# Performance work log

Measured on AMD Instinct MI355X. Metric: run time of the kernel, lower is better.

## Reference

```python
import math
import jax, jax.numpy as jnp
from jax import lax
import numpy as np

THETA = 10.0      # spiking threshold
TAU_SR = 10.0     # SRM (psp) alpha-kernel time constant
TAU_REF = 1.0     # refractory alpha-kernel time constant
SCALE_REF = 2.0   # refractory scale (kernel = -scaleRef*theta*alpha)
TAU_RHO = 1.0     # surrogate-gradient width
TS = 1.0          # simulation time step


def _alpha_filter_scan(x, tau, extra_input_fn=None):
    """Causal convolution along last (time) axis with alpha kernel
    k[n] = (n*Ts/tau) * exp(1 - n*Ts/tau)  (k[0] = 0),
    implemented exactly as a 2-state linear recurrence.
    x: [N, C, T] -> out: [N, C, T]."""
    d = jnp.float32(math.exp(-TS / tau))
    c = jnp.float32(math.e * TS / tau)
    xT = jnp.moveaxis(x, -1, 0)  # [T, N, C]

    def step(carry, xt):
        p, a = carry
        a = d * (a + p)          # alpha response from inputs up to t-1
        p = d * p + xt           # pure exponential state
        return (p, a), a * c

    z = jnp.zeros_like(xT[0])
    _, out = lax.scan(step, (z, z), xT)
    return jnp.moveaxis(out, 0, -1)


def psp(x):
    return _alpha_filter_scan(x, TAU_SR)


@jax.custom_vjp
def spike_fn(v):
    # Heaviside threshold on (membrane - theta)
    return (v >= 0).astype(v.dtype)

def _spike_fwd(v):
    return spike_fn(v), v

def _spike_bwd(v, g):
    # SLAYER surrogate gradient: exponential pdf around threshold
    grad = (1.0 / TAU_RHO) * jnp.exp(-jnp.abs(v) / TAU_RHO)
    return (g * grad,)

spike_fn.defvjp(_spike_fwd, _spike_bwd)


def spike_layer(u_in):
    """Threshold-and-refract over time. u_in: [N, C, T] psp potentials.
    Refractory response = -scaleRef*theta * alpha_{tauRef}(past spikes)."""
    d = jnp.float32(math.exp(-TS / TAU_REF))
    c = jnp.float32(math.e * TS / TAU_REF)
    ref_scale = jnp.float32(-SCALE_REF * THETA)
    uT = jnp.moveaxis(u_in, -1, 0)  # [T, N, C]

    def step(carry, ut):
        p, a = carry
        a = d * (a + p)                      # refractory potential at t
        u = ut + c * a                       # membrane potential
        s = spike_fn(u - THETA)              # spikes (0/1)
        p = d * p + ref_scale * s            # inject refractory impulse
        return (p, a), s

    z = jnp.zeros_like(uT[0])
    _, s = lax.scan(step, (z, z), uT)
    return jnp.moveaxis(s, 0, -1)


def setup_inputs() -> dict:
    key = jax.random.key(0)
    k1, k2, k3 = jax.random.split(key, 3)
    N, I, H, O, T = 64, 256, 1024, 18, 500
    # Bernoulli(0.1) input spikes
    spike_input = (jax.random.uniform(k1, (N, I, T)) < 0.1).astype(jnp.float32)
    W1 = jax.random.normal(k2, (H, I), dtype=jnp.float32) * (1.0 / math.sqrt(I))
    W2 = jax.random.normal(k3, (O, H), dtype=jnp.float32) * (1.0 / math.sqrt(H))
    return {"spike_input": spike_input, "W1": W1, "W2": W2}


def reference(spike_input, W1, W2):
    # layer 1: dense (per-timestep linear) -> psp -> spike
    y1 = jnp.einsum('nit,hi->nht', spike_input, W1)
    s1 = spike_layer(psp(y1))
    # layer 2
    y2 = jnp.einsum('nht,oh->not', s1, W2)
    s2 = spike_layer(psp(y2))
    return s2
```

## Files before the change

### kernel.cpp

```cpp
#include <hip/hip_runtime.h>


#define NN 64
#define II 256
#define HH 1024
#define OO 18
#define TT 500

#define D_SR 0.9048374180359595f
#define C_SR 0.27182818284590454f
#define D_RF 0.36787944117144233f
#define C_RF 2.718281828459045f
#define THETA 10.0f
#define REFS (-20.0f)

typedef _Float16 f16;
typedef _Float16 f16x8 __attribute__((ext_vector_type(8)));
typedef float f32x4 __attribute__((ext_vector_type(4)));

__device__ __forceinline__ void gl2lds16(const void* g, void* l) {
    __builtin_amdgcn_global_load_lds(
        (const __attribute__((address_space(1))) void*)g,
        (__attribute__((address_space(3))) void*)l, 16, 0, 0);
}

__launch_bounds__(256)
__global__ void prep_all(const float* __restrict__ X, const float* __restrict__ W1,
                         const float* __restrict__ W2, f16* __restrict__ Xb,
                         f16* __restrict__ W1h, f16* __restrict__ W1l,
                         f16* __restrict__ W2h, f16* __restrict__ W2l) {
    __shared__ float tile[64][65];
    const int b = blockIdx.x;
    const int tid = threadIdx.x;

    if (b < 2048) {
        const int t0 = (b & 7) * 64, i0 = ((b >> 3) & 3) * 64, n = b >> 5;
        const int tx = tid & 63, q = tid >> 6;
        const float* Xn = X + (size_t)n * II * TT;
#pragma unroll 4
        for (int j = 0; j < 16; ++j) {
            int il = j * 4 + q;
            int t = t0 + tx;
            tile[il][tx] = (t < TT) ? Xn[(size_t)(i0 + il) * TT + t] : 0.f;
        }
        __syncthreads();
#pragma unroll 4
        for (int j = 0; j < 16; ++j) {
            int tl = j * 4 + q;
            int t = t0 + tl;
            if (t < TT)
                Xb[((size_t)n * TT + t) * II + i0 + tx] = (f16)tile[tx][tl];
        }
    } else if (b < 3072) {
        int idx = (b - 2048) * 256 + tid;
        float w = W1[idx];
        f16 h = (f16)w;
        f16 l = (f16)(w - (float)h);
        W1h[idx] = h;
        W1l[idx] = l;
    } else {
        int idx = (b - 3072) * 256 + tid;
        int o = idx >> 10;
        float w = (o < OO) ? W2[idx] : 0.f;
        f16 h = (f16)w;
        f16 l = (f16)(w - (float)h);
        W2h[idx] = h;
        W2l[idx] = l;
    }
}

__launch_bounds__(512)
__global__ void gemm1_scan1(const f16* __restrict__ Xb, const f16* __restrict__ Wh,
                            const f16* __restrict__ Wl, f16* __restrict__ S1) {
    __shared__ __align__(16) char smem[128 * 132 * 4];
    float* yb = (float*)smem;

    const int tid = threadIdx.x;
    const int wave = tid >> 6, lane = tid & 63;

    const int f = blockIdx.y * 8 + blockIdx.x;
    const int x = f & 7, g = f >> 3;
    const int n = x * 8 + (g & 7);
    const int ht = g >> 3;
    const int h0g = ht * 128;

    const int rbl = wave * 16 + (lane >> 2);
    const int koff = (lane & 3) * 8;
    const f16* gBh0 = Wh + (size_t)(h0g + rbl) * II + koff;
    const f16* gBl0 = Wl + (size_t)(h0g + rbl) * II + koff;

    const int wm = wave & 1, wn = wave >> 1;
    const int fr = lane & 15, kq = lane >> 4;

    float p1 = 0.f, a1 = 0.f, p2 = 0.f, a2 = 0.f;

    for (int c = 0; c < 4; ++c) {
        const int t0 = c * 128;
        const int TCe = (TT - t0 < 128) ? (TT - t0) : 128;

        int r0 = rbl; if (r0 > TCe - 1) r0 = TCe - 1;
        const f16* gA0 = Xb + ((size_t)n * TT + t0 + r0) * II + koff;

        auto stage = [&](int kk2, int b) {
            f16* As_b = (f16*)(smem + b * 24576);
            f16* Bh_b = As_b + 4096;
            f16* Bl_b = As_b + 8192;
            const int ko = kk2 * 32;
            gl2lds16(gA0 + ko, As_b + wave * 512);
            gl2lds16(gBh0 + ko, Bh_b + wave * 512);
            gl2lds16(gBl0 + ko, Bl_b + wave * 512);
        };

        stage(0, 0);

        f32x4 acc[4][2] = {};
        for (int kk = 0; kk < 8; ++kk) {
            __syncthreads();
            if (kk < 7) stage(kk + 1, (kk + 1) & 1);

            const f16* As_b = (const f16*)(smem + (kk & 1) * 24576);
            const f16* Bh_b = As_b + 4096;
            const f16* Bl_b = As_b + 8192;

            f16x8 av[4], bhv[2], blv[2];
#pragma unroll
            for (int i = 0; i < 4; ++i)
                av[i] = *(const f16x8*)(As_b + (wm * 64 + i * 16 + fr) * 32 + kq * 8);
#pragma unroll
            for (int j = 0; j < 2; ++j) {
                bhv[j] = *(const f16x8*)(Bh_b + (wn * 32 + j * 16 + fr) * 32 + kq * 8);
                blv[j] = *(const f16x8*)(Bl_b + (wn * 32 + j * 16 + fr) * 32 + kq * 8);
            }
#pragma unroll
            for (int i = 0; i < 4; ++i)
#pragma unroll
                for (int j = 0; j < 2; ++j) {
                    acc[i][j] = __builtin_amdgcn_mfma_f32_16x16x32_f16(av[i], bhv[j], acc[i][j], 0, 0, 0);
                    acc[i][j] = __builtin_amdgcn_mfma_f32_16x16x32_f16(av[i], blv[j], acc[i][j], 0, 0, 0);
                }
        }
        __syncthreads();

#pragma unroll
        for (int i = 0; i < 4; ++i)
#pragma unroll
            for (int j = 0; j < 2; ++j) {
                int tr = wm * 64 + i * 16 + kq * 4;
                int hc = wn * 32 + j * 16 + fr;
#pragma unroll
                for (int r = 0; r < 4; ++r)
                    yb[(tr + r) * 132 + hc] = acc[i][j][r];
            }
        __syncthreads();

        if (tid < 128) {
            f16* sq = S1 + ((size_t)n * TT + t0) * HH + h0g + tid;
            float rb_[8];
#pragma unroll
            for (int j = 0; j < 8; ++j) rb_[j] = yb[j * 132 + tid];
            int t = 0;
            for (; t + 8 <= TCe; t += 8) {
#pragma unroll
                for (int j = 0; j < 8; ++j) {
                    float xv = rb_[j];
                    int tn = t + j + 8;
                    rb_[j] = (tn < TCe) ? yb[tn * 132 + tid] : 0.f;
                    a1 = D_SR * (a1 + p1);
                    p1 = D_SR * p1 + xv;
                    float ut = C_SR * a1;
                    a2 = D_RF * (a2 + p2);
                    float u = ut + C_RF * a2;
                    float s = (u >= THETA) ? 1.0f : 0.0f;
                    p2 = D_RF * p2 + REFS * s;
                    sq[(size_t)(t + j) * HH] = (f16)s;
                }
            }
            int rem = TCe - t;
#pragma unroll
            for (int j = 0; j < 8; ++j) {
                if (j < rem) {
                    float xv = rb_[j];
                    a1 = D_SR * (a1 + p1);
                    p1 = D_SR * p1 + xv;
                    float ut = C_SR * a1;
                    a2 = D_RF * (a2 + p2);
                    float u = ut + C_RF * a2;
                    float s = (u >= THETA) ? 1.0f : 0.0f;
                    p2 = D_RF * p2 + REFS * s;
                    sq[(size_t)(t + j) * HH] = (f16)s;
                }
            }
        }
        __syncthreads();
    }
}

__launch_bounds__(256)
__global__ void gemm2_mfma(const f16* __restrict__ S1, const f16* __restrict__ W2h,
                           const f16* __restrict__ W2l, float* __restrict__ Y2) {
    __shared__ __align__(16) f16 As[2][64 * 32];
    __shared__ __align__(16) f16 Bh[2][32 * 32];
    __shared__ __align__(16) f16 Bl[2][32 * 32];

    const int tid = threadIdx.x;
    const int wave = tid >> 6, lane = tid & 63;
    const int m0 = blockIdx.x * 64;
    const int fr = lane & 15, kq = lane >> 4;

    const f16* gA = S1 + (size_t)(m0 + wave * 16 + (lane >> 2)) * HH + (lane & 3) * 8;
    const f16* gB = (wave < 2 ? W2h : W2l) + (size_t)((wave & 1) * 16 + (lane >> 2)) * HH + (lane & 3) * 8;

    auto stage = [&](int kk2, int b) {
        const int ko = kk2 * 32;
        gl2lds16(gA + ko, &As[b][wave * 512]);
        gl2lds16(gB + ko, (wave < 2 ? &Bh[b][0] : &Bl[b][0]) + (wave & 1) * 512);
    };

    stage(0, 0);

    f32x4 acc[2] = {};
    for (int kk = 0; kk < HH / 32; ++kk) {
        __syncthreads();
        if (kk < HH / 32 - 1) stage(kk + 1, (kk + 1) & 1);
        const int b = kk & 1;

        f16x8 a, bh[2], bl[2];
        a = *(const f16x8*)(&As[b][(wave * 16 + fr) * 32 + kq * 8]);
#pragma unroll
        for (int j = 0; j < 2; ++j) {
            bh[j] = *(const f16x8*)(&Bh[b][(j * 16 + fr) * 32 + kq * 8]);
            bl[j] = *(const f16x8*)(&Bl[b][(j * 16 + fr) * 32 + kq * 8]);
        }
#pragma unroll
        for (int j = 0; j < 2; ++j) {
            acc[j] = __builtin_amdgcn_mfma_f32_16x16x32_f16(a, bh[j], acc[j], 0, 0, 0);
            acc[j] = __builtin_amdgcn_mfma_f32_16x16x32_f16(a, bl[j], acc[j], 0, 0, 0);
        }
    }

#pragma unroll
    for (int j = 0; j < 2; ++j) {
        int rbase = m0 + wave * 16 + kq * 4;
        int cc = j * 16 + fr;
        float* p = Y2 + (size_t)rbase * 32 + cc;
#pragma unroll
        for (int r = 0; r < 4; ++r)
            p[(size_t)r * 32] = acc[j][r];
    }
}

__launch_bounds__(256)
__global__ void scan2_k(const float* __restrict__ Y2, float* __restrict__ Out) {
    __shared__ float yc[TT * 32];
    __shared__ float sb[OO * TT];
    const int n = blockIdx.x, tid = threadIdx.x;

    const float4* src = (const float4*)(Y2 + (size_t)n * TT * 32);
    float4* dst = (float4*)yc;
    for (int i = tid; i < TT * 8; i += 256) dst[i] = src[i];
    __syncthreads();

    if (tid < 32) {
        float p1 = 0.f, a1 = 0.f, p2 = 0.f, a2 = 0.f;
        float rb_[8];
#pragma unroll
        for (int j = 0; j < 8; ++j) rb_[j] = yc[j * 32 + tid];
        int t = 0;
        for (; t + 8 <= TT; t += 8) {
#pragma unroll
            for (int j = 0; j < 8; ++j) {
                float xv = rb_[j];
                int tn = t + j + 8;
                rb_[j] = (tn < TT) ? yc[tn * 32 + tid] : 0.f;
                a1 = D_SR * (a1 + p1);
                p1 = D_SR * p1 + xv;
                float ut = C_SR * a1;
                a2 = D_RF * (a2 + p2);
                float u = ut + C_RF * a2;
                float s = (u >= THETA) ? 1.0f : 0.0f;
                p2 = D_RF * p2 + REFS * s;
                if (tid < OO) sb[tid * TT + t + j] = s;
            }
        }
#pragma unroll
        for (int j = 0; j < 8; ++j) {
            if (t + j < TT) {
                float xv = rb_[j];
                a1 = D_SR * (a1 + p1);
                p1 = D_SR * p1 + xv;
                float ut = C_SR * a1;
                a2 = D_RF * (a2 + p2);
                float u = ut + C_RF * a2;
                float s = (u >= THETA) ? 1.0f : 0.0f;
                p2 = D_RF * p2 + REFS * s;
                if (tid < OO) sb[tid * TT + t + j] = s;
            }
        }
    }
    __syncthreads();

    float* on = Out + (size_t)n * OO * TT;
    for (int e = tid; e < OO * TT; e += 256) on[e] = sb[e];
}

extern "C" void kernel_launch(void* const* d_in, const int* in_sizes, int n_in,
                              void* d_out, int out_size, void* d_ws, size_t ws_size,
                              hipStream_t stream) {
    const float* X  = (const float*)d_in[0];
    const float* W1 = (const float*)d_in[1];
    const float* W2 = (const float*)d_in[2];
    float* out = (float*)d_out;

    const size_t s_s1 = (size_t)NN * TT * HH * 2;
    const size_t s_Xb = (size_t)NN * TT * II * 2;
    const size_t s_W  = (size_t)HH * II * 2;
    const size_t s_W2 = (size_t)32 * HH * 2;

    char* w = (char*)d_ws;
    f16*   s1b = (f16*)w;  w += s_s1;
    f16*   Xb  = (f16*)w;  w += s_Xb;
    f16*   W1h = (f16*)w;  w += s_W;
    f16*   W1l = (f16*)w;  w += s_W;
    f16*   W2h = (f16*)w;  w += s_W2;
    f16*   W2l = (f16*)w;  w += s_W2;
    float* y2  = (float*)w;

    prep_all<<<3200, 256, 0, stream>>>(X, W1, W2, Xb, W1h, W1l, W2h, W2l);

    gemm1_scan1<<<dim3(8, NN), 512, 0, stream>>>(Xb, W1h, W1l, s1b);

    gemm2_mfma<<<(NN * TT) / 64, 256, 0, stream>>>(s1b, W2h, W2l, y2);
    scan2_k<<<NN, 256, 0, stream>>>(y2, out);
}
```

Baseline: 189.8 us.

## Pack layer-1 spikes into 64-bit ballot bitmasks instead of f16

```diff
diff --git a/kernel.cpp b/kernel.cpp
--- a/kernel.cpp
+++ b/kernel.cpp
@@ -17,6 +17,7 @@
 typedef _Float16 f16;
 typedef _Float16 f16x8 __attribute__((ext_vector_type(8)));
 typedef float f32x4 __attribute__((ext_vector_type(4)));
+typedef unsigned long long u64;
 
 __device__ __forceinline__ void gl2lds16(const void* g, void* l) {
     __builtin_amdgcn_global_load_lds(
@@ -71,7 +72,7 @@
 
 __launch_bounds__(512)
 __global__ void gemm1_scan1(const f16* __restrict__ Xb, const f16* __restrict__ Wh,
-                            const f16* __restrict__ Wl, f16* __restrict__ S1) {
+                            const f16* __restrict__ Wl, u64* __restrict__ Sb) {
     __shared__ __align__(16) char smem[128 * 132 * 4];
     float* yb = (float*)smem;
 
@@ -154,7 +155,7 @@
         __syncthreads();
 
         if (tid < 128) {
-            f16* sq = S1 + ((size_t)n * TT + t0) * HH + h0g + tid;
+            u64* sq = Sb + ((size_t)(n * TT + t0)) * 16 + ht * 2 + wave;
             float rb_[8];
 #pragma unroll
             for (int j = 0; j < 8; ++j) rb_[j] = yb[j * 132 + tid];
@@ -172,7 +173,8 @@
                     float u = ut + C_RF * a2;
                     float s = (u >= THETA) ? 1.0f : 0.0f;
                     p2 = D_RF * p2 + REFS * s;
-                    sq[(size_t)(t + j) * HH] = (f16)s;
+                    u64 bm = __ballot(u >= THETA);
+                    if (lane == 0) sq[(size_t)(t + j) * 16] = bm;
                 }
             }
             int rem = TCe - t;
@@ -187,7 +189,8 @@
                     float u = ut + C_RF * a2;
                     float s = (u >= THETA) ? 1.0f : 0.0f;
                     p2 = D_RF * p2 + REFS * s;
-                    sq[(size_t)(t + j) * HH] = (f16)s;
+                    u64 bm = __ballot(u >= THETA);
+                    if (lane == 0) sq[(size_t)(t + j) * 16] = bm;
                 }
             }
         }
@@ -196,9 +199,9 @@
 }
 
 __launch_bounds__(256)
-__global__ void gemm2_mfma(const f16* __restrict__ S1, const f16* __restrict__ W2h,
+__global__ void gemm2_mfma(const u64* __restrict__ Sb, const f16* __restrict__ W2h,
                            const f16* __restrict__ W2l, float* __restrict__ Y2) {
-    __shared__ __align__(16) f16 As[2][64 * 32];
+    __shared__ unsigned int bits[64 * 33];
     __shared__ __align__(16) f16 Bh[2][32 * 32];
     __shared__ __align__(16) f16 Bl[2][32 * 32];
 
@@ -207,25 +210,33 @@
     const int m0 = blockIdx.x * 64;
     const int fr = lane & 15, kq = lane >> 4;
 
-    const f16* gA = S1 + (size_t)(m0 + wave * 16 + (lane >> 2)) * HH + (lane & 3) * 8;
+    const unsigned int* g32 = (const unsigned int*)Sb + (size_t)m0 * 32;
+    for (int e = tid; e < 2048; e += 256)
+        bits[(e >> 5) * 33 + (e & 31)] = g32[e];
+
     const f16* gB = (wave < 2 ? W2h : W2l) + (size_t)((wave & 1) * 16 + (lane >> 2)) * HH + (lane & 3) * 8;
 
-    auto stage = [&](int kk2, int b) {
-        const int ko = kk2 * 32;
-        gl2lds16(gA + ko, &As[b][wave * 512]);
-        gl2lds16(gB + ko, (wave < 2 ? &Bh[b][0] : &Bl[b][0]) + (wave & 1) * 512);
+    auto stageB = [&](int kk2, int b) {
+        gl2lds16(gB + kk2 * 32, (wave < 2 ? &Bh[b][0] : &Bl[b][0]) + (wave & 1) * 512);
     };
 
-    stage(0, 0);
+    stageB(0, 0);
 
     f32x4 acc[2] = {};
+    const int brow = (wave * 16 + fr) * 33;
+    const f16 onef = (f16)1.0f, zerof = (f16)0.0f;
     for (int kk = 0; kk < HH / 32; ++kk) {
         __syncthreads();
-        if (kk < HH / 32 - 1) stage(kk + 1, (kk + 1) & 1);
+        if (kk < HH / 32 - 1) stageB(kk + 1, (kk + 1) & 1);
         const int b = kk & 1;
 
-        f16x8 a, bh[2], bl[2];
-        a = *(const f16x8*)(&As[b][(wave * 16 + fr) * 32 + kq * 8]);
+        unsigned int bw = bits[brow + kk];
+        f16x8 a;
+#pragma unroll
+        for (int j = 0; j < 8; ++j)
+            a[j] = ((bw >> (kq * 8 + j)) & 1u) ? onef : zerof;
+
+        f16x8 bh[2], bl[2];
 #pragma unroll
         for (int j = 0; j < 2; ++j) {
             bh[j] = *(const f16x8*)(&Bh[b][(j * 16 + fr) * 32 + kq * 8]);
@@ -311,13 +322,13 @@
     const float* W2 = (const float*)d_in[2];
     float* out = (float*)d_out;
 
-    const size_t s_s1 = (size_t)NN * TT * HH * 2;
+    const size_t s_sb = (size_t)NN * TT * 16 * 8;
     const size_t s_Xb = (size_t)NN * TT * II * 2;
     const size_t s_W  = (size_t)HH * II * 2;
     const size_t s_W2 = (size_t)32 * HH * 2;
 
     char* w = (char*)d_ws;
-    f16*   s1b = (f16*)w;  w += s_s1;
+    u64*   s1b = (u64*)w;  w += s_sb;
     f16*   Xb  = (f16*)w;  w += s_Xb;
     f16*   W1h = (f16*)w;  w += s_W;
     f16*   W1l = (f16*)w;  w += s_W;
```

New measurement: 192.7 us. Within noise of the previous version (+1.5%).
